# Optimization experiments

Measured on AMD Instinct MI355X. Metric: run time of the kernel, lower is better.

The kernel has to match this reference:

```python
import jax, jax.numpy as jnp
import numpy as np

C_LOGIT = 10.0  # logit clipping constant C from __init__
NEG_INF = -1e8


def setup_inputs() -> dict:
    key = jax.random.key(0)
    ks = jax.random.split(key, 10)
    B, S, E, H = 512, 256, 128, 128
    u = lambda k, sh: jax.random.uniform(k, sh, jnp.float32, -0.1, 0.1)
    return {
        "low_context_vector": jax.random.normal(ks[0], (B, S, E), jnp.float32),
        "original_node": jax.random.uniform(ks[1], (S, 2), jnp.float32),
        "mask": jnp.zeros((B, S), jnp.float32),
        # learned parameters
        "low_init_w": jax.random.uniform(ks[2], (2 * E,), jnp.float32, -1.0, 1.0),
        "Wc": u(ks[3], (E, E)),   "bc": u(ks[4], (E,)),     # low_h_context_embed
        "Wv": u(ks[5], (2 * E, E)), "bv": u(ks[6], (E,)),   # low_v_weight_embed
        "Wq": u(ks[7], (E, H)),                              # pointer query proj
        "Wref": u(ks[8], (E, H)),                            # pointer ref proj
        "v": u(ks[9], (H,)),                                 # pointer score vector
    }


def _decode(cv, mask, low_init_w, Wc, bc, Wv, bv, Wq, Wref, v, key):
    B, S, E = cv.shape
    h_bar = jnp.mean(cv, axis=1) @ Wc + bc              # [B,E]
    rest0 = low_init_w @ Wv + bv                        # [E]
    query0 = h_bar + rest0[None, :]                     # [B,E]
    ref = cv @ Wref                                     # [B,S,H], hoisted out of loop
    mask = mask.at[:, 0].set(1.0)                       # start node visited
    keys = jax.random.split(key, S - 1)
    binds = jnp.arange(B)

    def step(carry, k):
        mask, query, init_h, i = carry
        u_ = jnp.tanh((query @ Wq)[:, None, :] + ref) @ v      # [B,S]
        logits = jnp.where(mask > 0, NEG_INF, C_LOGIT * jnp.tanh(u_))
        logp = jax.nn.log_softmax(logits, axis=-1)
        g = jax.random.gumbel(k, logits.shape, logits.dtype)
        idx = jnp.argmax(logits + g, axis=-1)                  # Categorical sample, [B]
        lp = jnp.take_along_axis(logp, idx[:, None], axis=1)[:, 0]
        mask = mask.at[binds, idx].set(1.0)
        h = cv[binds, idx]                                     # gathered embedding [B,E]
        init_h = jnp.where(i == 0, h, init_h)                  # first pick cached
        query = h_bar + (jnp.concatenate([init_h, h], axis=-1) @ Wv + bv)
        return (mask, query, init_h, i + 1), (idx, lp)

    init = (mask, query0, jnp.zeros((B, E), cv.dtype), jnp.int32(0))
    _, (idxs, lps) = jax.lax.scan(step, init, keys)
    return idxs.T, lps.T  # [B, S-1] each


def reference(low_context_vector, original_node, mask, low_init_w, Wc, bc, Wv, bv, Wq, Wref, v):
    # original_node only feeds a printed local_reward in the torch code; it does
    # not affect the returned (indices, log_probs), so it is unused here.
    return _decode(low_context_vector, mask, low_init_w, Wc, bc, Wv, bv, Wq, Wref, v,
                   jax.random.key(42))
```

## Files before the change

kernel.cpp:

```cpp
#include <hip/hip_runtime.h>
#include <hip/hip_bf16.h>
#include <stdint.h>
#include <math.h>

#define NBATCH 512
#define NS 256
#define NE 128
#define NH 128
#define NSTEPS 255
#define NEGINF -1e8f
#define SENT_NEG -1e30f

__device__ __forceinline__ uint32_t rotl32(uint32_t x, uint32_t r) {
  return (x << r) | (x >> (32u - r));
}

__device__ __forceinline__ void tf2x32(uint32_t k0, uint32_t k1,
                                       uint32_t x0, uint32_t x1,
                                       uint32_t& o0, uint32_t& o1) {
  uint32_t ks2 = k0 ^ k1 ^ 0x1BD11BDAu;
  x0 += k0; x1 += k1;
#define TF_R4(a,b,c,d) \
  x0 += x1; x1 = rotl32(x1,a); x1 ^= x0; \
  x0 += x1; x1 = rotl32(x1,b); x1 ^= x0; \
  x0 += x1; x1 = rotl32(x1,c); x1 ^= x0; \
  x0 += x1; x1 = rotl32(x1,d); x1 ^= x0;
  TF_R4(13,15,26,6)   x0 += k1;  x1 += ks2 + 1u;
  TF_R4(17,29,16,24)  x0 += ks2; x1 += k0 + 2u;
  TF_R4(13,15,26,6)   x0 += k0;  x1 += k1 + 3u;
  TF_R4(17,29,16,24)  x0 += k1;  x1 += ks2 + 4u;
  TF_R4(13,15,26,6)   x0 += ks2; x1 += k0 + 5u;
#undef TF_R4
  o0 = x0; o1 = x1;
}

__device__ __forceinline__ float gumbel_of(uint2 key, uint32_t j) {
  uint32_t o0, o1;
  tf2x32(key.x, key.y, 0u, j, o0, o1);
  uint32_t bits = o0 ^ o1;
  float f = __uint_as_float((bits >> 9) | 0x3f800000u) - 1.0f;
  float u = (f == 0.0f) ? 1.17549435e-38f : f;
  float l1 = -logf(u);
  return -logf(l1);
}

__device__ __forceinline__ float nr_tanh(float x) {
  const float Chi = 2.8853900432586670f;
  const float Clo = 3.8519259822379735e-08f;
  float m = fmaf(x, Chi, x * Clo);
  m = fminf(m, 126.0f);
  float tt = __builtin_amdgcn_exp2f(m);
  float d  = tt + 1.0f;
  float r  = __builtin_amdgcn_rcpf(d);
  r = r * fmaf(-d, r, 2.0f);
  return fmaf(-2.0f, r, 1.0f);
}

__device__ __forceinline__ double dot32(const float4* __restrict__ a,
                                        const float4* __restrict__ bp) {
  double s = 0.0;
#pragma unroll
  for (int q = 0; q < 8; ++q) {
    float4 x = a[q], y = bp[q];
    s += (double)x.x * (double)y.x + (double)x.y * (double)y.y
       + (double)x.z * (double)y.z + (double)x.w * (double)y.w;
  }
  return s;
}

__device__ __forceinline__ double dot4d(float4 a, float4 b) {
  return ((double)a.x * (double)b.x + (double)a.y * (double)b.y)
       + ((double)a.z * (double)b.z + (double)a.w * (double)b.w);
}

__global__ void k1_mats(const float* __restrict__ Wv, const float* __restrict__ Wq,
                        const float* __restrict__ liw, const float* __restrict__ bvv,
                        float* __restrict__ M1T, float* __restrict__ M2T,
                        float* __restrict__ rest0) {
  int e = blockIdx.x, h = threadIdx.x;
  __shared__ float wrow[NE];
  if (e < 256) {
    wrow[h] = Wv[e * NE + h];
    __syncthreads();
    double a = 0.0;
    for (int k = 0; k < NE; ++k) a += (double)wrow[k] * (double)Wq[k * NH + h];
    if (e < 128) M1T[h * NE + e] = (float)a;
    else         M2T[h * NE + (e - 128)] = (float)a;
  } else {
    double a = 0.0;
    for (int k = 0; k < 2 * NE; ++k) a += (double)liw[k] * (double)Wv[k * NE + h];
    rest0[h] = (float)a + bvv[h];
  }
}

__global__ void k2_base(const float* __restrict__ cv, const float* __restrict__ Wc,
                        const float* __restrict__ bc, const float* __restrict__ bvv,
                        const float* __restrict__ Wq, const float* __restrict__ rest0,
                        double* __restrict__ qqbase, float* __restrict__ qq0) {
  int b = blockIdx.x, h = threadIdx.x;
  int b256 = b << 8;
  __shared__ float meanL[NE], hbarL[NE];
  double ms = 0.0;
  for (int s = 0; s < NS; ++s) ms += (double)cv[((size_t)b256 + s) * NE + h];
  meanL[h] = (float)(ms * (1.0 / 256.0));
  __syncthreads();
  double a = 0.0;
  for (int e = 0; e < NE; ++e) a += (double)meanL[e] * (double)Wc[e * NE + h];
  hbarL[h] = (float)a + bc[h];
  __syncthreads();
  double ab = 0.0, a0 = 0.0;
  for (int k = 0; k < NE; ++k) {
    double w = (double)Wq[k * NH + h];
    ab += (double)(hbarL[k] + bvv[k]) * w;
    a0 += (double)(hbarL[k] + rest0[k]) * w;
  }
  qqbase[(size_t)b * NH + h] = ab;
  qq0[(size_t)b * NH + h] = (float)a0;
}

__global__ __launch_bounds__(256, 4)
void k_a2v3(const float* __restrict__ cv, const float* __restrict__ M2T,
            double* __restrict__ A2) {
  const int b  = blockIdx.x >> 3;
  const int s0 = (blockIdx.x & 7) << 5;
  const int t  = threadIdx.x;
  const int h  = t >> 1;
  const int kh = t & 1;
  const int b256 = b << 8;
  __shared__ float cvS[32][132];
  for (int idx = t; idx < 32 * NE; idx += 256) {
    int r = idx >> 7, c = idx & 127;
    cvS[r][c] = cv[((size_t)(b256 + s0 + r)) * NE + c];
  }
  __syncthreads();
  float4 m2r[16];
  {
    const float4* m2p = (const float4*)(M2T + (size_t)h * NE + kh * 64);
#pragma unroll
    for (int q = 0; q < 16; ++q) m2r[q] = m2p[q];
  }
#pragma unroll 2
  for (int sLoc = 0; sLoc < 32; ++sLoc) {
    const float4* cr4 = ((const float4*)&cvS[sLoc][0]) + kh * 16;
    double c0 = 0.0, c1 = 0.0;
#pragma unroll
    for (int q = 0; q < 16; q += 2) {
      c0 += dot4d(cr4[q],     m2r[q]);
      c1 += dot4d(cr4[q + 1], m2r[q + 1]);
    }
    double s = c0 + c1;
    s += __shfl_xor(s, 1, 64);
    if (kh == 0)
      A2[((size_t)(b256 + s0 + sLoc)) * NH + h] = s;
  }
}

struct MainSh {
  alignas(16) float  qq[NH];
  alignas(16) float  vvf[NH];
  float  logitArr[NS];
  alignas(8)  double base128[NH];
  uint2  keyL[NSTEPS];
  float  redV[8];
  float  redS[8];
  int    redI[8];
};

struct PreSh {
  float cvS[NS][33];
  float wS[32][NH];
};

template <int MODE>
__global__ __launch_bounds__(512, 4)
void decode_main(const float* __restrict__ cv,
                 const float* __restrict__ mask_in,
                 const float* __restrict__ Wref,
                 const float* __restrict__ vvec,
                 const double* __restrict__ qqbase,
                 const float* __restrict__ M1T,
                 const float* __restrict__ M2T,
                 const float* __restrict__ qq0,
                 const double* __restrict__ A2,
                 float* __restrict__ out) {
  const int b = blockIdx.x;
  const int t = threadIdx.x;
  const int b256 = b << 8;
  const int w = t >> 6, l = t & 63;
  const int i = (w << 5) | (l >> 1);
  const int hHalf = l & 1;
  const int hb = hHalf << 6;

  __shared__ union { PreSh pre; MainSh m; } sh;
  __shared__ short rowIdA[NS], rowIdB[NS], posA[NS], posB[NS];
  __shared__ int nActSh[2], jSh[2], tmp8[4];
  __shared__ alignas(16) float refScratch[NE];

  bool act0 = false;
  if (t < NS) {
    act0 = !((t == 0) || (mask_in[(size_t)b256 + t] > 0.0f));
    uint64_t mb = __ballot(act0);
    int lane = t & 63, wv = t >> 6;
    int pre = __popcll(mb & (((uint64_t)1 << lane) - 1));
    if (lane == 0) tmp8[wv] = (int)__popcll(mb);
    posA[t] = (short)pre;
  }
  __syncthreads();
  if (t < NS) {
    int base = 0;
    for (int k = 0; k < (t >> 6); ++k) base += tmp8[k];
    int p = base + (int)posA[t];
    if (act0) rowIdA[p] = (short)t;
    posA[t] = (short)p;
  }
  if (t == 0) {
    nActSh[0] = tmp8[0] + tmp8[1] + tmp8[2] + tmp8[3];
    jSh[0] = -1;
  }
  __syncthreads();
  const int nAct0 = nActSh[0];

  const int myRow0 = (i < nAct0) ? (int)rowIdA[i] : 0;
  float refr[64];
#pragma unroll
  for (int j = 0; j < 64; ++j) refr[j] = 0.0f;

  for (int ec = 0; ec < 4; ++ec) {
    __syncthreads();
    for (int ii = t; ii < 32 * NH; ii += 512) {
      int r = ii >> 7, c = ii & 127;
      sh.pre.wS[r][c] = Wref[(ec * 32 + r) * NH + c];
    }
    for (int ii = t; ii < NS * 32; ii += 512) {
      int r = ii >> 5, c = ii & 31;
      sh.pre.cvS[r][c] = cv[((size_t)b256 + r) * NE + ec * 32 + c];
    }
    __syncthreads();
    for (int hc = 0; hc < 8; ++hc) {
      double a[8] = {0,0,0,0,0,0,0,0};
      for (int e = 0; e < 32; ++e) {
        double cd = (double)sh.pre.cvS[myRow0][e];
        const float* wp = &sh.pre.wS[e][hb + hc * 8];
#pragma unroll
        for (int j = 0; j < 8; ++j) a[j] += cd * (double)wp[j];
      }
#pragma unroll
      for (int j = 0; j < 8; ++j) refr[hc * 8 + j] += (float)a[j];
    }
  }
  __syncthreads();

  if (t < NSTEPS) {
    uint32_t o0, o1;
    tf2x32(0u, 42u, 0u, (uint32_t)t, o0, o1);
    sh.m.keyL[t] = make_uint2(o0, o1);
  }
  if (t < NH) {
    sh.m.vvf[t] = vvec[t];
    sh.m.qq[t] = qq0[(size_t)b * NH + t];
  }
  __syncthreads();

  float g = 0.0f;
  if (i < nAct0)
    g = gumbel_of(sh.m.keyL[0], (uint32_t)(b256 + myRow0));

  for (int step = 0; step < NSTEPS; ++step) {
    const int cur = step & 1;
    const short* rowId_c = cur ? rowIdB : rowIdA;
    const short* pos_c   = cur ? posB   : posA;
    short* rowId_n = cur ? rowIdA : rowIdB;
    short* pos_n   = cur ? posA   : posB;
    const int nA    = nActSh[cur];
    const int jPrev = jSh[cur];
    const bool active = (i < nA);
    const int myRow = active ? (int)rowId_c[i] : 0;

    if (jPrev >= 0 && i == jPrev) {
      const float4* rs4 = (const float4*)(refScratch + hb);
#pragma unroll
      for (int q = 0; q < 16; ++q) {
        float4 v4 = rs4[q];
        refr[4 * q + 0] = v4.x; refr[4 * q + 1] = v4.y;
        refr[4 * q + 2] = v4.z; refr[4 * q + 3] = v4.w;
      }
    }

    double accH = 0.0;
    if (active) {
      double a0 = 0, a1 = 0, a2 = 0, a3 = 0;
      const float4* qq4 = (const float4*)(sh.m.qq + hb);
      const float4* vv4 = (const float4*)(sh.m.vvf + hb);
#pragma unroll
      for (int q = 0; q < 16; ++q) {
        float4 qv = qq4[q];
        float4 wv = vv4[q];
        a0 += (double)nr_tanh(qv.x + refr[4 * q + 0]) * (double)wv.x;
        a1 += (double)nr_tanh(qv.y + refr[4 * q + 1]) * (double)wv.y;
        a2 += (double)nr_tanh(qv.z + refr[4 * q + 2]) * (double)wv.z;
        a3 += (double)nr_tanh(qv.w + refr[4 * q + 3]) * (double)wv.w;
      }
      accH = (a0 + a1) + (a2 + a3);
    }
    double other = __shfl_xor(accH, 1, 64);
    float val = SENT_NEG; int vRow = 0x7fffffff; float term = 0.0f;
    if (active) {
      double tot = hHalf ? (other + accH) : (accH + other);
      float u_ = (float)tot;
      float logit = 10.0f * (float)tanh((double)u_);
      if (!hHalf) {
        sh.m.logitArr[myRow] = logit;
        term = expf(logit);
      }
      val = logit + g;
      vRow = myRow;
    }

    float bvv = val; int bR = vRow; float bss = term;
#pragma unroll
    for (int mm = 1; mm <= 32; mm <<= 1) {
      float ov = __shfl_xor(bvv, mm, 64);
      int   oR = __shfl_xor(bR,  mm, 64);
      float os = __shfl_xor(bss, mm, 64);
      bss += os;
      if (ov > bvv || (ov == bvv && oR < bR)) { bvv = ov; bR = oR; }
    }

    double pf0 = 0.0, pf1 = 0.0;
    bool havePf = false;
    if (MODE == 1 && step > 0 && step + 1 < NSTEPS && (unsigned)bR <= 255u) {
      const double* ap = A2 + (size_t)(b256 + bR) * NH + (l << 1);
      pf0 = ap[0]; pf1 = ap[1];
      havePf = true;
    }

    if (l == 0) { sh.m.redV[w] = bvv; sh.m.redI[w] = bR; sh.m.redS[w] = bss; }
    __syncthreads();

    float BV = sh.m.redV[0]; int BR = sh.m.redI[0];
#pragma unroll
    for (int k = 1; k < 8; ++k) {
      float ov = sh.m.redV[k]; int oR = sh.m.redI[k];
      if (ov > BV || (ov == BV && oR < BR)) { BV = ov; BR = oR; }
    }
    if ((unsigned)BR > 255u) BR = 0;
    const int BI = BR;
    const int jj = (int)pos_c[BI];

    if (t == 0) {
      float SS = (sh.m.redS[0] + sh.m.redS[1]) + (sh.m.redS[2] + sh.m.redS[3]);
      SS += (sh.m.redS[4] + sh.m.redS[5]) + (sh.m.redS[6] + sh.m.redS[7]);
      float lp = sh.m.logitArr[BI] - (float)log((double)SS);
      out[(size_t)b * NSTEPS + step] = (float)BI;
      out[(size_t)NBATCH * NSTEPS + (size_t)b * NSTEPS + step] = lp;
      nActSh[cur ^ 1] = nA - 1;
      jSh[cur ^ 1] = (jj < nA - 1) ? jj : -1;
    }

    if (t < NS) {
      int donorRow = (int)rowId_c[nA - 1];
      short rid = (t == jj) ? (short)donorRow : rowId_c[t];
      rowId_n[t] = rid;
      if (t < nA - 1) pos_n[rid] = (short)t;
    }
    if (jj < nA - 1 && i == nA - 1) {
      float4* rs4 = (float4*)(refScratch + hb);
#pragma unroll
      for (int q = 0; q < 16; ++q)
        rs4[q] = make_float4(refr[4 * q + 0], refr[4 * q + 1],
                             refr[4 * q + 2], refr[4 * q + 3]);
    }

    if (step + 1 < NSTEPS && i < nA - 1) {
      int ridN = (i == jj) ? (int)rowId_c[nA - 1] : myRow;
      g = gumbel_of(sh.m.keyL[step + 1], (uint32_t)(b256 + ridN));
    }

    if (step + 1 < NSTEPS) {
      if (MODE == 1) {
        if (step == 0) {
          const int hq = t >> 2, kq = t & 3;
          const float4* hrow = (const float4*)(cv + (size_t)(b256 + BI) * NE + kq * 32);
          const float4* m1p  = (const float4*)(M1T + (size_t)hq * NE + kq * 32);
          double am = dot32(hrow, m1p);
          am += __shfl_xor(am, 1, 64);
          am += __shfl_xor(am, 2, 64);
          if (kq == 0) {
            double dbase = qqbase[(size_t)b * NH + hq] + am;
            sh.m.base128[hq] = dbase;
            sh.m.qq[hq] = (float)(dbase + A2[(size_t)(b256 + BI) * NH + hq]);
          }
        } else if (havePf && bR == BI) {
          const int h0 = l << 1;
          sh.m.qq[h0]     = (float)(sh.m.base128[h0]     + pf0);
          sh.m.qq[h0 + 1] = (float)(sh.m.base128[h0 + 1] + pf1);
        }
      } else {
        const int hq = t >> 2, kq = t & 3;
        const float4* hrow = (const float4*)(cv + (size_t)(b256 + BI) * NE + kq * 32);
        const float4* m2p  = (const float4*)(M2T + (size_t)hq * NE + kq * 32);
        double a2 = dot32(hrow, m2p);
        a2 += __shfl_xor(a2, 1, 64);
        a2 += __shfl_xor(a2, 2, 64);
        if (step == 0) {
          const float4* m1p = (const float4*)(M1T + (size_t)hq * NE + kq * 32);
          double am = dot32(hrow, m1p);
          am += __shfl_xor(am, 1, 64);
          am += __shfl_xor(am, 2, 64);
          if (kq == 0) {
            double dbase = qqbase[(size_t)b * NH + hq] + am;
            sh.m.base128[hq] = dbase;
            sh.m.qq[hq] = (float)(dbase + a2);
          }
        } else if (kq == 0) {
          sh.m.qq[hq] = (float)(sh.m.base128[hq] + a2);
        }
      }
    }
    __syncthreads();
  }
}

__device__ __forceinline__ float fast_tanh_ref(float x) {
  const float Chi = 2.8853900432586670f;
  const float Clo = 3.8519259822379735e-08f;
  float m = fmaf(x, Chi, x * Clo);
  float tt = exp2f(m);
  return 1.0f - 2.0f / (tt + 1.0f);
}

struct MainShR {
  float  query[NE];
  float  qq[NH];
  float  hbar[NE];
  float  inith[NE];
  float  hcur[NE];
  alignas(16) double vvd[NH];
  float  logitArr[NS];
  float  maskArr[NS];
  uint2  keyL[NSTEPS];
  float  meanv[NE];
  float  redV[4];
  int    redI[4];
  double redS[4];
  int    idxSh;
};
struct PreShR {
  float cvS[NS][33];
  float wS[32][NH];
};

__global__ __launch_bounds__(256, 2)
void decoder_kernel_ref(const float* __restrict__ cv, const float* __restrict__ mask_in,
                        const float* __restrict__ liw, const float* __restrict__ Wc,
                        const float* __restrict__ bc, const float* __restrict__ Wv,
                        const float* __restrict__ bv, const float* __restrict__ Wq,
                        const float* __restrict__ Wref, const float* __restrict__ vvec,
                        float* __restrict__ out) {
  const int b = blockIdx.x;
  const int t = threadIdx.x;
  const int b256 = b << 8;
  __shared__ union { PreShR pre; MainShR m; } sh;

  float refr[NH];
#pragma unroll
  for (int h = 0; h < NH; ++h) refr[h] = 0.0f;
  for (int ec = 0; ec < 4; ++ec) {
    const int e0 = ec * 32;
    __syncthreads();
    for (int i = t; i < 32 * NH; i += 256) {
      int r = i >> 7, h = i & 127;
      sh.pre.wS[r][h] = Wref[(e0 + r) * NH + h];
    }
    for (int i = t; i < NS * 32; i += 256) {
      int s2 = i >> 5, j = i & 31;
      sh.pre.cvS[s2][j] = cv[((size_t)b256 + s2) * NE + e0 + j];
    }
    __syncthreads();
#pragma unroll
    for (int hc = 0; hc < 16; ++hc) {
      double a[8] = {0,0,0,0,0,0,0,0};
      for (int e = 0; e < 32; ++e) {
        double cd = (double)sh.pre.cvS[t][e];
#pragma unroll
        for (int j = 0; j < 8; ++j) a[j] += cd * (double)sh.pre.wS[e][hc * 8 + j];
      }
#pragma unroll
      for (int j = 0; j < 8; ++j) refr[hc * 8 + j] += (float)a[j];
    }
  }
  __syncthreads();

  if (t < NSTEPS) {
    uint32_t o0, o1;
    tf2x32(0u, 42u, 0u, (uint32_t)t, o0, o1);
    sh.m.keyL[t] = make_uint2(o0, o1);
  }
  if (t < NH) sh.m.vvd[t] = (double)vvec[t];
  sh.m.maskArr[t] = (mask_in[(size_t)b256 + t] > 0.0f || t == 0) ? 1.0f : 0.0f;
  if (t < NE) {
    double s64 = 0.0;
    for (int s2 = 0; s2 < NS; ++s2) s64 += (double)cv[((size_t)b256 + s2) * NE + t];
    sh.m.meanv[t] = (float)(s64 * (1.0 / 256.0));
  }
  __syncthreads();
  if (t < NE) {
    double acc = 0.0;
    for (int e = 0; e < NE; ++e) acc += (double)sh.m.meanv[e] * (double)Wc[e * NE + t];
    float hbv = (float)acc + bc[t];
    sh.m.hbar[t] = hbv;
    double acc2 = 0.0;
    for (int k = 0; k < 2 * NE; ++k) acc2 += (double)liw[k] * (double)Wv[k * NE + t];
    float r0 = (float)acc2 + bv[t];
    sh.m.query[t] = hbv + r0;
  }
  __syncthreads();

  for (int step = 0; step < NSTEPS; ++step) {
    if (t < NH) {
      double acc = 0.0;
      for (int k = 0; k < NE; ++k) acc += (double)sh.m.query[k] * (double)Wq[k * NH + t];
      sh.m.qq[t] = (float)acc;
    }
    __syncthreads();

    float logit;
    bool masked = (sh.m.maskArr[t] != 0.0f);
    if (!masked) {
      double a0 = 0.0, a1 = 0.0, a2 = 0.0, a3 = 0.0;
      const float4*  qq4 = (const float4*)sh.m.qq;
      const double2* vv2 = (const double2*)sh.m.vvd;
#pragma unroll
      for (int h4 = 0; h4 < 32; ++h4) {
        float4  q  = qq4[h4];
        double2 va = vv2[2 * h4];
        double2 vb = vv2[2 * h4 + 1];
        a0 += (double)fast_tanh_ref(q.x + refr[4 * h4 + 0]) * va.x;
        a1 += (double)fast_tanh_ref(q.y + refr[4 * h4 + 1]) * va.y;
        a2 += (double)fast_tanh_ref(q.z + refr[4 * h4 + 2]) * vb.x;
        a3 += (double)fast_tanh_ref(q.w + refr[4 * h4 + 3]) * vb.y;
      }
      float u_ = (float)((a0 + a1) + (a2 + a3));
      logit = 10.0f * (float)tanh((double)u_);
    } else {
      logit = NEGINF;
    }
    sh.m.logitArr[t] = logit;

    uint2 key = sh.m.keyL[step];
    uint32_t j = (uint32_t)(b256 + t);
    uint32_t o0, o1;
    tf2x32(key.x, key.y, 0u, j, o0, o1);
    uint32_t bits = o0 ^ o1;
    float f = __uint_as_float((bits >> 9) | 0x3f800000u) - 1.0f;
    float u = (f == 0.0f) ? 1.17549435e-38f : f;
    float l1 = (float)(-log((double)u));
    float g  = (float)(-log((double)l1));
    float val = logit + g;
    double term = exp((double)logit);

    float bv_ = val; int bi = t; double bs = term;
#pragma unroll
    for (int m = 1; m <= 32; m <<= 1) {
      float  ov = __shfl_xor(bv_, m, 64);
      int    oi = __shfl_xor(bi,  m, 64);
      double os = __shfl_xor(bs,  m, 64);
      if (ov > bv_ || (ov == bv_ && oi < bi)) { bv_ = ov; bi = oi; }
      bs += os;
    }
    int w = t >> 6;
    if ((t & 63) == 0) { sh.m.redV[w] = bv_; sh.m.redI[w] = bi; sh.m.redS[w] = bs; }
    __syncthreads();

    if (t == 0) {
      float BV = sh.m.redV[0]; int BI = sh.m.redI[0];
      for (int k = 1; k < 4; ++k) {
        float ov = sh.m.redV[k]; int oi = sh.m.redI[k];
        if (ov > BV || (ov == BV && oi < BI)) { BV = ov; BI = oi; }
      }
      double SS = ((sh.m.redS[0] + sh.m.redS[1]) + (sh.m.redS[2] + sh.m.redS[3]));
      sh.m.idxSh = BI;
      float lp = sh.m.logitArr[BI] - (float)log(SS);
      out[(size_t)b * NSTEPS + step] = (float)BI;
      out[(size_t)NBATCH * NSTEPS + (size_t)b * NSTEPS + step] = lp;
    }
    __syncthreads();

    int idx = sh.m.idxSh;
    if (t == idx) sh.m.maskArr[t] = 1.0f;
    if (t < NE) {
      float hc = cv[((size_t)b256 + idx) * NE + t];
      sh.m.hcur[t] = hc;
      if (step == 0) sh.m.inith[t] = hc;
    }
    __syncthreads();

    if (t < NE) {
      double acc2 = 0.0;
      for (int k = 0; k < NE; ++k) acc2 += (double)sh.m.inith[k] * (double)Wv[k * NE + t];
      for (int k = 0; k < NE; ++k) acc2 += (double)sh.m.hcur[k] * (double)Wv[(NE + k) * NE + t];
      float mm = (float)acc2 + bv[t];
      sh.m.query[t] = sh.m.hbar[t] + mm;
    }
    __syncthreads();
  }
}

extern "C" void kernel_launch(void* const* d_in, const int* in_sizes, int n_in,
                              void* d_out, int out_size, void* d_ws, size_t ws_size,
                              hipStream_t stream) {
  const float* cv   = (const float*)d_in[0];
  const float* mask = (const float*)d_in[2];
  const float* liw  = (const float*)d_in[3];
  const float* Wc   = (const float*)d_in[4];
  const float* bc   = (const float*)d_in[5];
  const float* Wv   = (const float*)d_in[6];
  const float* bv   = (const float*)d_in[7];
  const float* Wq   = (const float*)d_in[8];
  const float* Wref = (const float*)d_in[9];
  const float* vv   = (const float*)d_in[10];
  (void)in_sizes; (void)n_in; (void)out_size;

  const size_t SZ_QQB = (size_t)NBATCH * NH * sizeof(double);
  const size_t SZ_M   = (size_t)NE * NH * sizeof(float);
  const size_t SZ_QQ0 = (size_t)NBATCH * NH * sizeof(float);
  const size_t SZ_A2  = (size_t)NBATCH * NS * NH * sizeof(double);
  const size_t need_min = SZ_QQB + 2 * SZ_M + SZ_QQ0 + 512;
  const size_t need_pre = need_min + SZ_A2;

  if (ws_size >= need_min) {
    char* p = (char*)d_ws;
    double* qqbase = (double*)p;            p += SZ_QQB;
    float*  M1T    = (float*)p;             p += SZ_M;
    float*  M2T    = (float*)p;             p += SZ_M;
    float*  qq0    = (float*)p;             p += SZ_QQ0;
    float*  rest0  = (float*)p;             p += 512;
    double* A2     = (double*)p;

    k1_mats<<<257, 128, 0, stream>>>(Wv, Wq, liw, bv, M1T, M2T, rest0);
    k2_base<<<NBATCH, 128, 0, stream>>>(cv, Wc, bc, bv, Wq, rest0, qqbase, qq0);
    if (ws_size >= need_pre) {
      k_a2v3<<<NBATCH * 8, 256, 0, stream>>>(cv, M2T, A2);
      decode_main<1><<<NBATCH, 512, 0, stream>>>(cv, mask, Wref, vv, qqbase, M1T,
                                                 M2T, qq0, A2, (float*)d_out);
    } else {
      decode_main<0><<<NBATCH, 512, 0, stream>>>(cv, mask, Wref, vv, qqbase, M1T,
                                                 M2T, qq0, nullptr, (float*)d_out);
    }
  } else {
    decoder_kernel_ref<<<NBATCH, 256, 0, stream>>>(cv, mask, liw, Wc, bc, Wv, bv,
                                                   Wq, Wref, vv, (float*)d_out);
  }
}
```

Measured before the change: 3.029 ms.

## Cut decode loop to one barrier per step with implicit compaction and double-buffered reductions

```diff
diff --git a/kernel.cpp b/kernel.cpp
--- a/kernel.cpp
+++ b/kernel.cpp
@@ -155,15 +155,17 @@
   }
 }
 
-struct MainSh {
+struct MainSh1 {
   alignas(16) float  qq[NH];
   alignas(16) float  vvf[NH];
   float  logitArr[NS];
   alignas(8)  double base128[NH];
   uint2  keyL[NSTEPS];
-  float  redV[8];
-  float  redS[8];
-  int    redI[8];
+  float  redV[2][8];
+  float  redS[2][8];
+  int    redI[2][8];
+  alignas(16) float refScr[2][NE];
+  int    sRowId[2];
 };
 
 struct PreSh {
@@ -171,18 +173,16 @@
   float wS[32][NH];
 };
 
-template <int MODE>
 __global__ __launch_bounds__(512, 4)
-void decode_main(const float* __restrict__ cv,
-                 const float* __restrict__ mask_in,
-                 const float* __restrict__ Wref,
-                 const float* __restrict__ vvec,
-                 const double* __restrict__ qqbase,
-                 const float* __restrict__ M1T,
-                 const float* __restrict__ M2T,
-                 const float* __restrict__ qq0,
-                 const double* __restrict__ A2,
-                 float* __restrict__ out) {
+void decode_1b(const float* __restrict__ cv,
+               const float* __restrict__ mask_in,
+               const float* __restrict__ Wref,
+               const float* __restrict__ vvec,
+               const double* __restrict__ qqbase,
+               const float* __restrict__ M1T,
+               const float* __restrict__ qq0,
+               const double* __restrict__ A2,
+               float* __restrict__ out) {
   const int b = blockIdx.x;
   const int t = threadIdx.x;
   const int b256 = b << 8;
@@ -190,37 +190,31 @@
   const int i = (w << 5) | (l >> 1);
   const int hHalf = l & 1;
   const int hb = hHalf << 6;
-
-  __shared__ union { PreSh pre; MainSh m; } sh;
-  __shared__ short rowIdA[NS], rowIdB[NS], posA[NS], posB[NS];
-  __shared__ int nActSh[2], jSh[2], tmp8[4];
-  __shared__ alignas(16) float refScratch[NE];
-
-  bool act0 = false;
+  const int h0 = l << 1;
+
+  __shared__ union { PreSh pre; MainSh1 m; } sh;
+  __shared__ short rowId0[NS];
+  __shared__ int tmp8[4], nActSh0;
+
+  bool act0 = false; int preCnt = 0;
   if (t < NS) {
     act0 = !((t == 0) || (mask_in[(size_t)b256 + t] > 0.0f));
     uint64_t mb = __ballot(act0);
     int lane = t & 63, wv = t >> 6;
-    int pre = __popcll(mb & (((uint64_t)1 << lane) - 1));
+    preCnt = __popcll(mb & (((uint64_t)1 << lane) - 1));
     if (lane == 0) tmp8[wv] = (int)__popcll(mb);
-    posA[t] = (short)pre;
-  }
-  __syncthreads();
-  if (t < NS) {
+  }
+  __syncthreads();
+  if (t < NS && act0) {
     int base = 0;
     for (int k = 0; k < (t >> 6); ++k) base += tmp8[k];
-    int p = base + (int)posA[t];
-    if (act0) rowIdA[p] = (short)t;
-    posA[t] = (short)p;
-  }
-  if (t == 0) {
-    nActSh[0] = tmp8[0] + tmp8[1] + tmp8[2] + tmp8[3];
-    jSh[0] = -1;
-  }
-  __syncthreads();
-  const int nAct0 = nActSh[0];
-
-  const int myRow0 = (i < nAct0) ? (int)rowIdA[i] : 0;
+    rowId0[base + preCnt] = (short)t;
+  }
+  if (t == 0) nActSh0 = tmp8[0] + tmp8[1] + tmp8[2] + tmp8[3];
+  __syncthreads();
+  const int nAct0 = nActSh0;
+
+  int myRow = (i < nAct0) ? (int)rowId0[i] : 0;
   float refr[64];
 #pragma unroll
   for (int j = 0; j < 64; ++j) refr[j] = 0.0f;
@@ -239,7 +233,7 @@
     for (int hc = 0; hc < 8; ++hc) {
       double a[8] = {0,0,0,0,0,0,0,0};
       for (int e = 0; e < 32; ++e) {
-        double cd = (double)sh.pre.cvS[myRow0][e];
+        double cd = (double)sh.pre.cvS[myRow][e];
         const float* wp = &sh.pre.wS[e][hb + hc * 8];
 #pragma unroll
         for (int j = 0; j < 8; ++j) a[j] += cd * (double)wp[j];
@@ -263,27 +257,32 @@
 
   float g = 0.0f;
   if (i < nAct0)
-    g = gumbel_of(sh.m.keyL[0], (uint32_t)(b256 + myRow0));
+    g = gumbel_of(sh.m.keyL[0], (uint32_t)(b256 + myRow));
+  bool adoptNext = false;
 
   for (int step = 0; step < NSTEPS; ++step) {
-    const int cur = step & 1;
-    const short* rowId_c = cur ? rowIdB : rowIdA;
-    const short* pos_c   = cur ? posB   : posA;
-    short* rowId_n = cur ? rowIdA : rowIdB;
-    short* pos_n   = cur ? posA   : posB;
-    const int nA    = nActSh[cur];
-    const int jPrev = jSh[cur];
+    const int par = step & 1;
+    const int nA = nAct0 - step;
     const bool active = (i < nA);
-    const int myRow = active ? (int)rowId_c[i] : 0;
-
-    if (jPrev >= 0 && i == jPrev) {
-      const float4* rs4 = (const float4*)(refScratch + hb);
+
+    if (adoptNext) {
+      myRow = sh.m.sRowId[par ^ 1];
+      const float4* rs4 = (const float4*)(&sh.m.refScr[par ^ 1][hb]);
 #pragma unroll
       for (int q = 0; q < 16; ++q) {
         float4 v4 = rs4[q];
         refr[4 * q + 0] = v4.x; refr[4 * q + 1] = v4.y;
         refr[4 * q + 2] = v4.z; refr[4 * q + 3] = v4.w;
       }
+      adoptNext = false;
+    }
+    if (active && i == nA - 1) {
+      float4* rs4 = (float4*)(&sh.m.refScr[par][hb]);
+#pragma unroll
+      for (int q = 0; q < 16; ++q)
+        rs4[q] = make_float4(refr[4 * q + 0], refr[4 * q + 1],
+                             refr[4 * q + 2], refr[4 * q + 3]);
+      sh.m.sRowId[par] = myRow;
     }
 
     double accH = 0.0;
@@ -303,7 +302,7 @@
       accH = (a0 + a1) + (a2 + a3);
     }
     double other = __shfl_xor(accH, 1, 64);
-    float val = SENT_NEG; int vRow = 0x7fffffff; float term = 0.0f;
+    float val = SENT_NEG; int bR = 0x7fffffff; float term = 0.0f;
     if (active) {
       double tot = hHalf ? (other + accH) : (accH + other);
       float u_ = (float)tot;
@@ -313,10 +312,10 @@
         term = expf(logit);
       }
       val = logit + g;
-      vRow = myRow;
-    }
-
-    float bvv = val; int bR = vRow; float bss = term;
+      bR = myRow;
+    }
+
+    float bvv = val; float bss = term;
 #pragma unroll
     for (int mm = 1; mm <= 32; mm <<= 1) {
       float ov = __shfl_xor(bvv, mm, 64);
@@ -326,98 +325,71 @@
       if (ov > bvv || (ov == bvv && oR < bR)) { bvv = ov; bR = oR; }
     }
 
-    double pf0 = 0.0, pf1 = 0.0;
-    bool havePf = false;
-    if (MODE == 1 && step > 0 && step + 1 < NSTEPS && (unsigned)bR <= 255u) {
-      const double* ap = A2 + (size_t)(b256 + bR) * NH + (l << 1);
-      pf0 = ap[0]; pf1 = ap[1];
-      havePf = true;
-    }
-
-    if (l == 0) { sh.m.redV[w] = bvv; sh.m.redI[w] = bR; sh.m.redS[w] = bss; }
-    __syncthreads();
-
-    float BV = sh.m.redV[0]; int BR = sh.m.redI[0];
+    const bool waveNext = ((w << 5) < nA - 1) && (step + 1 < NSTEPS);
+
+    double pf0 = 0.0, pf1 = 0.0; bool havePf = false;
+    if (waveNext && step > 0 && (unsigned)bR <= 255u) {
+      const double* ap = A2 + (size_t)(b256 + bR) * NH + h0;
+      pf0 = ap[0]; pf1 = ap[1]; havePf = true;
+    }
+
+    if (l == 0) {
+      sh.m.redV[par][w] = bvv; sh.m.redI[par][w] = bR; sh.m.redS[par][w] = bss;
+    }
+    __syncthreads();
+
+    float BV = sh.m.redV[par][0]; int BR_ = sh.m.redI[par][0];
 #pragma unroll
     for (int k = 1; k < 8; ++k) {
-      float ov = sh.m.redV[k]; int oR = sh.m.redI[k];
-      if (ov > BV || (ov == BV && oR < BR)) { BV = ov; BR = oR; }
-    }
-    if ((unsigned)BR > 255u) BR = 0;
-    const int BI = BR;
-    const int jj = (int)pos_c[BI];
+      float ov = sh.m.redV[par][k]; int oR = sh.m.redI[par][k];
+      if (ov > BV || (ov == BV && oR < BR_)) { BV = ov; BR_ = oR; }
+    }
+    if ((unsigned)BR_ > 255u) BR_ = 0;
+    const int BI = BR_;
 
     if (t == 0) {
-      float SS = (sh.m.redS[0] + sh.m.redS[1]) + (sh.m.redS[2] + sh.m.redS[3]);
-      SS += (sh.m.redS[4] + sh.m.redS[5]) + (sh.m.redS[6] + sh.m.redS[7]);
+      float SS = (sh.m.redS[par][0] + sh.m.redS[par][1]) + (sh.m.redS[par][2] + sh.m.redS[par][3]);
+      SS += (sh.m.redS[par][4] + sh.m.redS[par][5]) + (sh.m.redS[par][6] + sh.m.redS[par][7]);
       float lp = sh.m.logitArr[BI] - (float)log((double)SS);
       out[(size_t)b * NSTEPS + step] = (float)BI;
       out[(size_t)NBATCH * NSTEPS + (size_t)b * NSTEPS + step] = lp;
-      nActSh[cur ^ 1] = nA - 1;
-      jSh[cur ^ 1] = (jj < nA - 1) ? jj : -1;
-    }
-
-    if (t < NS) {
-      int donorRow = (int)rowId_c[nA - 1];
-      short rid = (t == jj) ? (short)donorRow : rowId_c[t];
-      rowId_n[t] = rid;
-      if (t < nA - 1) pos_n[rid] = (short)t;
-    }
-    if (jj < nA - 1 && i == nA - 1) {
-      float4* rs4 = (float4*)(refScratch + hb);
-#pragma unroll
-      for (int q = 0; q < 16; ++q)
-        rs4[q] = make_float4(refr[4 * q + 0], refr[4 * q + 1],
-                             refr[4 * q + 2], refr[4 * q + 3]);
-    }
+    }
+
+    adoptNext = active && (myRow == BI) && (i != nA - 1);
 
     if (step + 1 < NSTEPS && i < nA - 1) {
-      int ridN = (i == jj) ? (int)rowId_c[nA - 1] : myRow;
+      int ridN = adoptNext ? sh.m.sRowId[par] : myRow;
       g = gumbel_of(sh.m.keyL[step + 1], (uint32_t)(b256 + ridN));
     }
 
-    if (step + 1 < NSTEPS) {
-      if (MODE == 1) {
-        if (step == 0) {
-          const int hq = t >> 2, kq = t & 3;
-          const float4* hrow = (const float4*)(cv + (size_t)(b256 + BI) * NE + kq * 32);
-          const float4* m1p  = (const float4*)(M1T + (size_t)hq * NE + kq * 32);
-          double am = dot32(hrow, m1p);
-          am += __shfl_xor(am, 1, 64);
-          am += __shfl_xor(am, 2, 64);
-          if (kq == 0) {
-            double dbase = qqbase[(size_t)b * NH + hq] + am;
-            sh.m.base128[hq] = dbase;
-            sh.m.qq[hq] = (float)(dbase + A2[(size_t)(b256 + BI) * NH + hq]);
-          }
-        } else if (havePf && bR == BI) {
-          const int h0 = l << 1;
-          sh.m.qq[h0]     = (float)(sh.m.base128[h0]     + pf0);
-          sh.m.qq[h0 + 1] = (float)(sh.m.base128[h0 + 1] + pf1);
-        }
-      } else {
+    if (step == 0) {
+      if (NSTEPS > 1) {
         const int hq = t >> 2, kq = t & 3;
         const float4* hrow = (const float4*)(cv + (size_t)(b256 + BI) * NE + kq * 32);
-        const float4* m2p  = (const float4*)(M2T + (size_t)hq * NE + kq * 32);
-        double a2 = dot32(hrow, m2p);
-        a2 += __shfl_xor(a2, 1, 64);
-        a2 += __shfl_xor(a2, 2, 64);
-        if (step == 0) {
-          const float4* m1p = (const float4*)(M1T + (size_t)hq * NE + kq * 32);
-          double am = dot32(hrow, m1p);
-          am += __shfl_xor(am, 1, 64);
-          am += __shfl_xor(am, 2, 64);
-          if (kq == 0) {
-            double dbase = qqbase[(size_t)b * NH + hq] + am;
-            sh.m.base128[hq] = dbase;
-            sh.m.qq[hq] = (float)(dbase + a2);
-          }
-        } else if (kq == 0) {
-          sh.m.qq[hq] = (float)(sh.m.base128[hq] + a2);
+        const float4* m1p  = (const float4*)(M1T + (size_t)hq * NE + kq * 32);
+        double am = dot32(hrow, m1p);
+        am += __shfl_xor(am, 1, 64);
+        am += __shfl_xor(am, 2, 64);
+        if (kq == 0)
+          sh.m.base128[hq] = qqbase[(size_t)b * NH + hq] + am;
+        __syncthreads();
+        if (waveNext) {
+          double a0v = A2[(size_t)(b256 + BI) * NH + h0];
+          double a1v = A2[(size_t)(b256 + BI) * NH + h0 + 1];
+          sh.m.qq[h0]     = (float)(sh.m.base128[h0]     + a0v);
+          sh.m.qq[h0 + 1] = (float)(sh.m.base128[h0 + 1] + a1v);
         }
       }
-    }
-    __syncthreads();
+    } else if (waveNext) {
+      double a0v, a1v;
+      if (havePf && bR == BI) { a0v = pf0; a1v = pf1; }
+      else {
+        a0v = A2[(size_t)(b256 + BI) * NH + h0];
+        a1v = A2[(size_t)(b256 + BI) * NH + h0 + 1];
+      }
+      sh.m.qq[h0]     = (float)(sh.m.base128[h0]     + a0v);
+      sh.m.qq[h0 + 1] = (float)(sh.m.base128[h0 + 1] + a1v);
+    }
   }
 }
 
@@ -625,10 +597,9 @@
   const size_t SZ_M   = (size_t)NE * NH * sizeof(float);
   const size_t SZ_QQ0 = (size_t)NBATCH * NH * sizeof(float);
   const size_t SZ_A2  = (size_t)NBATCH * NS * NH * sizeof(double);
-  const size_t need_min = SZ_QQB + 2 * SZ_M + SZ_QQ0 + 512;
-  const size_t need_pre = need_min + SZ_A2;
-
-  if (ws_size >= need_min) {
+  const size_t need_pre = SZ_QQB + 2 * SZ_M + SZ_QQ0 + 512 + SZ_A2;
+
+  if (ws_size >= need_pre) {
     char* p = (char*)d_ws;
     double* qqbase = (double*)p;            p += SZ_QQB;
     float*  M1T    = (float*)p;             p += SZ_M;
@@ -639,14 +610,9 @@
 
     k1_mats<<<257, 128, 0, stream>>>(Wv, Wq, liw, bv, M1T, M2T, rest0);
     k2_base<<<NBATCH, 128, 0, stream>>>(cv, Wc, bc, bv, Wq, rest0, qqbase, qq0);
-    if (ws_size >= need_pre) {
-      k_a2v3<<<NBATCH * 8, 256, 0, stream>>>(cv, M2T, A2);
-      decode_main<1><<<NBATCH, 512, 0, stream>>>(cv, mask, Wref, vv, qqbase, M1T,
-                                                 M2T, qq0, A2, (float*)d_out);
-    } else {
-      decode_main<0><<<NBATCH, 512, 0, stream>>>(cv, mask, Wref, vv, qqbase, M1T,
-                                                 M2T, qq0, nullptr, (float*)d_out);
-    }
+    k_a2v3<<<NBATCH * 8, 256, 0, stream>>>(cv, M2T, A2);
+    decode_1b<<<NBATCH, 512, 0, stream>>>(cv, mask, Wref, vv, qqbase, M1T,
+                                          qq0, A2, (float*)d_out);
   } else {
     decoder_kernel_ref<<<NBATCH, 256, 0, stream>>>(cv, mask, liw, Wc, bc, Wv, bv,
                                                    Wq, Wref, vv, (float*)d_out);
```

After: 3.065 ms. Within noise of the previous version (+1.2%).
